# Kernel optimization log

Hardware: AMD Instinct MI355X
Metric: run time of the kernel (lower is better)

The kernel has to match this reference:

```python
import jax, jax.numpy as jnp
import numpy as np

N_FACES = 50000
C_IN = 256
C_OUT = 256
K = 9  # kernel_size ** 2
PAD_SIZE = N_FACES + 1


def _pad_features(x, face_is_pad):
    # Faithful to: padded_x = zeros(pad_size, C); padded_x[~face_is_pad] = x
    # rank[i] = position of row i among the non-pad slots (in order)
    rank = jnp.cumsum(~face_is_pad) - 1            # [P]
    rank = jnp.clip(rank, 0, x.shape[0] - 1)
    padded = jnp.where(face_is_pad[:, None], jnp.zeros((), x.dtype), x[rank])
    return padded                                   # [P, C_in]


def setup_inputs() -> dict:
    key = jax.random.key(0)
    k1, k2, k3 = jax.random.split(key, 3)
    x = jax.random.normal(k1, (N_FACES, C_IN), dtype=jnp.float32)
    weight = jax.random.normal(k2, (C_OUT, C_IN, 1, K), dtype=jnp.float32)
    bias = jnp.zeros((C_OUT,), dtype=jnp.float32)
    face_neighborhood = jax.random.randint(k3, (N_FACES, K), 0, PAD_SIZE, dtype=jnp.int64)
    # exactly one pad slot (the last one); sum(~face_is_pad) == N_FACES == x.shape[0]
    face_is_pad = jnp.zeros((PAD_SIZE,), dtype=bool).at[PAD_SIZE - 1].set(True)
    return {"x": x, "weight": weight, "bias": bias,
            "face_neighborhood": face_neighborhood,
            "face_is_pad": face_is_pad, "pad_size": PAD_SIZE}


def reference(x, weight, bias, face_neighborhood, face_is_pad, pad_size):
    # demodulation: per-output-channel L2 normalization of the weight
    dcoefs = jax.lax.rsqrt(jnp.sum(weight * weight, axis=(1, 2, 3)) + 1e-8)  # [O]
    w = weight * dcoefs[:, None, None, None]        # [O, I, 1, K]
    padded = _pad_features(x, face_is_pad)          # [P, I]
    gathered = padded[face_neighborhood]            # [N, K, I]
    # 1x9 conv over gathered neighbors == contraction over (I, K)
    out = jnp.einsum('nki,oik->no', gathered, w[:, :, 0, :]) + bias  # [N, O]
    return out
```

## Files before the change

### kernel.cpp

```cpp
#include <hip/hip_runtime.h>

#define NF    50000
#define PADP  50001
#define KN    9
#define KTOT  2304
#define NCHUNK 782
#define BM2   256
#define NBLK2 196
#define NKT   36
#define BUF   65536
#define BOFF  32768
#define IDXOFF2 131072

#define WT_OFF   0u
#define FLAG_OFF 1179648u
#define CNT_OFF  1179904u
#define PADX_OFF 1183744u

typedef float f32x4 __attribute__((ext_vector_type(4)));
typedef __bf16 bf16x8 __attribute__((ext_vector_type(8)));

typedef const __attribute__((address_space(1))) unsigned int* gas_t;
typedef __attribute__((address_space(3))) unsigned int* las_t;

static __device__ __forceinline__ void gll16(const void* g, void* l) {
  __builtin_amdgcn_global_load_lds((gas_t)g, (las_t)l, 16, 0, 0);
}

static __device__ __forceinline__ unsigned short f2bf(float f) {
  unsigned int u = __builtin_bit_cast(unsigned int, f);
  u = u + 0x7fffu + ((u >> 16) & 1u);
  return (unsigned short)(u >> 16);
}


__global__ void k_prep(const float* __restrict__ w, unsigned short* __restrict__ wt,
                       const unsigned char* __restrict__ pad, int* __restrict__ cnt,
                       const unsigned int* __restrict__ raw, int* __restrict__ flag) {
  if (blockIdx.x < 256) {
    int o = blockIdx.x;
    int i = threadIdx.x;
    const float* wr = w + (o * 256 + i) * 9;
    float wv[9];
    float s = 0.f;
#pragma unroll
    for (int k = 0; k < 9; ++k) { wv[k] = wr[k]; s += wv[k] * wv[k]; }
#pragma unroll
    for (int d = 32; d >= 1; d >>= 1) s += __shfl_xor(s, d);
    __shared__ float red[4];
    if ((i & 63) == 0) red[i >> 6] = s;
    __syncthreads();
    float dc = rsqrtf(red[0] + red[1] + red[2] + red[3] + 1e-8f);
#pragma unroll
    for (int k = 0; k < 9; ++k)
      wt[o * KTOT + k * 256 + i] = f2bf(wv[k] * dc);
  } else {
    int cb = blockIdx.x - 256;
    int t = cb * 256 + threadIdx.x;
    bool ip = (t < PADP) ? (pad[t] != 0) : true;
    unsigned long long m = __ballot(ip);
    int c = t >> 6;
    if ((threadIdx.x & 63) == 0 && c < NCHUNK) cnt[c] = __popcll(m);
    if (cb == 0 && threadIdx.x < 64) {
      unsigned int v = raw[threadIdx.x * 2 + 1];
      unsigned long long nz = __ballot(v != 0u);
      if (threadIdx.x == 0) flag[0] = (nz == 0ull) ? 1 : 0;
    }
  }
}

__global__ __launch_bounds__(256) void k_rankpadx(
    const float* __restrict__ x, const unsigned char* __restrict__ pad,
    const int* __restrict__ cnt, unsigned short* __restrict__ padx) {
  const int c = blockIdx.x;
  const int tid = threadIdx.x, w = tid >> 6, lane = tid & 63;
  int s = 0;
  for (int i = tid; i < c; i += 256) s += cnt[i];
#pragma unroll
  for (int d = 32; d >= 1; d >>= 1) s += __shfl_xor(s, d);
  __shared__ int red[4];
  __shared__ int rnk[64];
  if (lane == 0) red[w] = s;
  __syncthreads();
  const int S = red[0] + red[1] + red[2] + red[3];
  if (w == 0) {
    int p = c * 64 + lane;
    bool ip = (p < PADP) ? (pad[p] != 0) : true;
    unsigned long long m = __ballot(ip);
    int before = __popcll(m & ((1ull << lane) - 1ull));
    rnk[lane] = ip ? -1 : (p - (S + before));
  }
  __syncthreads();
  const int col = lane * 4;
#pragma unroll
  for (int i = 0; i < 16; ++i) {
    int rl = i * 4 + w;
    int pp = c * 64 + rl;
    if (pp >= PADP) continue;
    int rr = rnk[rl];
    ushort4 ov;
    if (rr < 0) { ov.x = 0; ov.y = 0; ov.z = 0; ov.w = 0; }
    else {
      const float4 v = *(const float4*)(x + rr * 256 + col);
      ov.x = f2bf(v.x); ov.y = f2bf(v.y); ov.z = f2bf(v.z); ov.w = f2bf(v.w);
    }
    *(ushort4*)(padx + pp * 256 + col) = ov;
  }
}

__global__ __launch_bounds__(512, 2) void k_main(
    const unsigned short* __restrict__ padx,
    const unsigned short* __restrict__ wt,
    const void* __restrict__ nbr,
    const int* __restrict__ flag,
    const float* __restrict__ bias,
    float* __restrict__ out) {
  __shared__ __align__(16) unsigned char sm[140288];
  const int tid = threadIdx.x;
  const int wv = tid >> 6, lane = tid & 63;
  const int m0 = blockIdx.x * BM2;
  int* idxl = (int*)(sm + IDXOFF2);

  const int q = lane & 15, hi = lane >> 4;
  const int wm = wv >> 2, wn = wv & 3;

  float bv[4];
#pragma unroll
  for (int ni = 0; ni < 4; ++ni) bv[ni] = bias[wn * 64 + ni * 16 + q];

  const bool f64 = (flag[0] != 0);
  const long long* n64 = (const long long*)nbr;
  const int* n32 = (const int*)nbr;
  for (int e = tid; e < BM2 * 9; e += 512) {
    int f = m0 + e / 9;
    if (f >= NF) f = NF - 1;
    int k = e - (e / 9) * 9;
    idxl[e] = f64 ? (int)n64[f * KN + k] : n32[f * KN + k];
  }
  __syncthreads();

  const int swsrc = ((tid & 7) ^ ((tid >> 3) & 7)) * 8;
  const int fl0 = tid >> 3;
  const int rb0 = fl0 * 9, rb1 = (fl0 + 64) * 9, rb2 = (fl0 + 128) * 9, rb3 = (fl0 + 192) * 9;
  const unsigned short* wtb00 = wt + (fl0      ) * KTOT + swsrc;
  const unsigned short* wtb01 = wt + (fl0 +  64) * KTOT + swsrc;
  const unsigned short* wtb10 = wt + (fl0 + 128) * KTOT + swsrc;
  const unsigned short* wtb11 = wt + (fl0 + 192) * KTOT + swsrc;

  const int q7 = q & 7;
  const int aof0 = wm * 16384 + q * 128 + ((hi    ) ^ q7) * 16;
  const int aof1 = wm * 16384 + q * 128 + ((4 + hi) ^ q7) * 16;
  const int bof0 = BOFF + (wn * 64 + q) * 128 + ((hi    ) ^ q7) * 16;
  const int bof1 = BOFF + (wn * 64 + q) * 128 + ((4 + hi) ^ q7) * 16;

  f32x4 acc[8][4];
#pragma unroll
  for (int a = 0; a < 8; ++a)
#pragma unroll
    for (int b = 0; b < 4; ++b) {
      acc[a][b][0] = 0.f; acc[a][b][1] = 0.f; acc[a][b][2] = 0.f; acc[a][b][3] = 0.f;
    }

  bf16x8 af[8], bq[4];
  int pA0 = idxl[rb0], pA1 = idxl[rb1], pA2 = idxl[rb2], pA3 = idxl[rb3];

  gll16(wtb00, sm + BOFF + tid * 16);
  gll16(wtb01, sm + BOFF + 8192 + tid * 16);
  gll16(wtb10, sm + BOFF + 16384 + tid * 16);
  gll16(wtb11, sm + BOFF + 24576 + tid * 16);
  gll16(padx + pA0 * 256 + swsrc, sm + tid * 16);
  gll16(padx + pA1 * 256 + swsrc, sm + 8192 + tid * 16);
  gll16(padx + pA2 * 256 + swsrc, sm + 16384 + tid * 16);
  gll16(padx + pA3 * 256 + swsrc, sm + 24576 + tid * 16);
  gll16(wtb00 + 64, sm + BUF + BOFF + tid * 16);
  gll16(wtb01 + 64, sm + BUF + BOFF + 8192 + tid * 16);
  gll16(wtb10 + 64, sm + BUF + BOFF + 16384 + tid * 16);
  gll16(wtb11 + 64, sm + BUF + BOFF + 24576 + tid * 16);
  asm volatile("s_waitcnt vmcnt(0)" ::: "memory");
  __builtin_amdgcn_s_barrier();

#define LD(p) (*(const bf16x8*)(p))
#define SB __builtin_amdgcn_sched_barrier(0);
#define MF(MI, AFI) \
  acc[MI][0] = __builtin_amdgcn_mfma_f32_16x16x32_bf16(af[AFI], bq[0], acc[MI][0], 0,0,0); \
  acc[MI][1] = __builtin_amdgcn_mfma_f32_16x16x32_bf16(af[AFI], bq[1], acc[MI][1], 0,0,0); \
  acc[MI][2] = __builtin_amdgcn_mfma_f32_16x16x32_bf16(af[AFI], bq[2], acc[MI][2], 0,0,0); \
  acc[MI][3] = __builtin_amdgcn_mfma_f32_16x16x32_bf16(af[AFI], bq[3], acc[MI][3], 0,0,0);
#define TAIL(M0,M1,M2,M3) \
  SB __builtin_amdgcn_s_barrier(); \
  asm volatile("s_waitcnt lgkmcnt(0)" ::: "memory"); SB \
  __builtin_amdgcn_s_setprio(1); \
  MF(M0,M0) MF(M1,M1) MF(M2,M2) MF(M3,M3) \
  __builtin_amdgcn_s_setprio(0); \
  SB __builtin_amdgcn_s_barrier();

#define PH0(CUR,OTH,C0A) { \
  const unsigned char* cb = sm + (CUR)*BUF; \
  af[0]=LD(cb+aof0); af[1]=LD(cb+aof0+2048); af[2]=LD(cb+aof0+4096); af[3]=LD(cb+aof0+6144); \
  bq[0]=LD(cb+bof0); bq[1]=LD(cb+bof0+2048); bq[2]=LD(cb+bof0+4096); bq[3]=LD(cb+bof0+6144); \
  gll16(padx + pA0*256 + (C0A) + swsrc, sm + (OTH)*BUF + tid*16); \
  gll16(padx + pA1*256 + (C0A) + swsrc, sm + (OTH)*BUF + 8192 + tid*16); \
  TAIL(0,1,2,3) }

#define PH1(CUR,OTH,C0A) { \
  const unsigned char* cb = sm + (CUR)*BUF; \
  af[4]=LD(cb+aof0+8192); af[5]=LD(cb+aof0+10240); af[6]=LD(cb+aof0+12288); af[7]=LD(cb+aof0+14336); \
  gll16(padx + pA2*256 + (C0A) + swsrc, sm + (OTH)*BUF + 16384 + tid*16); \
  gll16(padx + pA3*256 + (C0A) + swsrc, sm + (OTH)*BUF + 24576 + tid*16); \
  TAIL(4,5,6,7) }

#define PH2(CUR, DOREF) { \
  const unsigned char* cb = sm + (CUR)*BUF; \
  af[0]=LD(cb+aof1); af[1]=LD(cb+aof1+2048); af[2]=LD(cb+aof1+4096); af[3]=LD(cb+aof1+6144); \
  bq[0]=LD(cb+bof1); bq[1]=LD(cb+bof1+2048); bq[2]=LD(cb+bof1+4096); bq[3]=LD(cb+bof1+6144); \
  if (DOREF) { int gn = g4 + 1; if (gn > 8) gn = 8; \
    pA0 = idxl[rb0+gn]; pA1 = idxl[rb1+gn]; pA2 = idxl[rb2+gn]; pA3 = idxl[rb3+gn]; } \
  TAIL(0,1,2,3) }

#define PH3(CUR, KB) { \
  const unsigned char* cb = sm + (CUR)*BUF; \
  af[4]=LD(cb+aof1+8192); af[5]=LD(cb+aof1+10240); af[6]=LD(cb+aof1+12288); af[7]=LD(cb+aof1+14336); \
  gll16(wtb00 + (KB), sm + (CUR)*BUF + BOFF + tid*16); \
  gll16(wtb01 + (KB), sm + (CUR)*BUF + BOFF + 8192 + tid*16); \
  gll16(wtb10 + (KB), sm + (CUR)*BUF + BOFF + 16384 + tid*16); \
  gll16(wtb11 + (KB), sm + (CUR)*BUF + BOFF + 24576 + tid*16); \
  asm volatile("s_waitcnt vmcnt(4)" ::: "memory"); \
  TAIL(4,5,6,7) }

#pragma unroll 1
  for (int g4 = 0; g4 < 9; ++g4) {
    const int ktb = g4 * 4;
    int u;
    PH0(0,1,64) PH1(0,1,64) PH2(0,0)
    u = ktb + 2; if (u > 35) u = 35;
    PH3(0, u*64)
    PH0(1,0,128) PH1(1,0,128) PH2(1,0)
    u = ktb + 3; if (u > 35) u = 35;
    PH3(1, u*64)
    PH0(0,1,192) PH1(0,1,192) PH2(0,1)
    u = ktb + 4; if (u > 35) u = 35;
    PH3(0, u*64)
    PH0(1,0,0) PH1(1,0,0) PH2(1,0)
    u = ktb + 5; if (u > 35) u = 35;
    PH3(1, u*64)
  }
#undef PH0
#undef PH1
#undef PH2
#undef PH3
#undef TAIL
#undef MF
#undef LD
#undef SB
  asm volatile("s_waitcnt vmcnt(0)" ::: "memory");

#pragma unroll
  for (int ni = 0; ni < 4; ++ni) {
    const int col = wn * 64 + ni * 16 + q;
#pragma unroll
    for (int mi = 0; mi < 8; ++mi) {
#pragma unroll
      for (int rr = 0; rr < 4; ++rr) {
        const int row = m0 + wm * 128 + mi * 16 + hi * 4 + rr;
        if (row < NF) out[row * 256 + col] = acc[mi][ni][rr] + bv[ni];
      }
    }
  }
}

extern "C" void kernel_launch(void* const* d_in, const int* in_sizes, int n_in,
                              void* d_out, int out_size, void* d_ws, size_t ws_size,
                              hipStream_t stream) {
  const float* x = (const float*)d_in[0];
  const float* wfull = (const float*)d_in[1];
  const float* bias = (const float*)d_in[2];
  const void* nbr = d_in[3];
  const unsigned char* pad = (const unsigned char*)d_in[4];
  float* out = (float*)d_out;
  char* ws = (char*)d_ws;

  unsigned short* wt   = (unsigned short*)(ws + WT_OFF);
  int* flag            = (int*)(ws + FLAG_OFF);
  int* cnt             = (int*)(ws + CNT_OFF);
  unsigned short* padx = (unsigned short*)(ws + PADX_OFF);

  k_prep<<<452, 256, 0, stream>>>(wfull, wt, pad, cnt, (const unsigned int*)nbr, flag);
  k_rankpadx<<<NCHUNK, 256, 0, stream>>>(x, pad, cnt, padx);
  k_main<<<NBLK2, 512, 0, stream>>>(padx, wt, nbr, flag, bias, out);
}
```

Measured before the change: 87.68 us.

## Load weight fragments directly from global into registers, drop weight LDS staging

The weight (B) operand is no longer staged through LDS via global_load_lds. Each lane now reads its bf16 weight fragments straight from global memory into registers, double-buffered across half-k-steps. This halves the LDS footprint, which could allow more blocks per CU, and removes the LDS writes and reads for B. In exchange it issues more global loads per wave, relies on L2/L1 hits for the shared weights, and uses a hand-tuned vmcnt wait that must account for the new loads.

```diff
diff --git a/kernel.cpp b/kernel.cpp
--- a/kernel.cpp
+++ b/kernel.cpp
@@ -8,9 +8,8 @@
 #define BM2   256
 #define NBLK2 196
 #define NKT   36
-#define BUF   65536
-#define BOFF  32768
-#define IDXOFF2 131072
+#define BUF   32768
+#define IDXOFF2 65536
 
 #define WT_OFF   0u
 #define FLAG_OFF 1179648u
@@ -115,7 +114,7 @@
     const int* __restrict__ flag,
     const float* __restrict__ bias,
     float* __restrict__ out) {
-  __shared__ __align__(16) unsigned char sm[140288];
+  __shared__ __align__(16) unsigned char sm[74752];
   const int tid = threadIdx.x;
   const int wv = tid >> 6, lane = tid & 63;
   const int m0 = blockIdx.x * BM2;
@@ -142,16 +141,15 @@
   const int swsrc = ((tid & 7) ^ ((tid >> 3) & 7)) * 8;
   const int fl0 = tid >> 3;
   const int rb0 = fl0 * 9, rb1 = (fl0 + 64) * 9, rb2 = (fl0 + 128) * 9, rb3 = (fl0 + 192) * 9;
-  const unsigned short* wtb00 = wt + (fl0      ) * KTOT + swsrc;
-  const unsigned short* wtb01 = wt + (fl0 +  64) * KTOT + swsrc;
-  const unsigned short* wtb10 = wt + (fl0 + 128) * KTOT + swsrc;
-  const unsigned short* wtb11 = wt + (fl0 + 192) * KTOT + swsrc;
 
   const int q7 = q & 7;
   const int aof0 = wm * 16384 + q * 128 + ((hi    ) ^ q7) * 16;
   const int aof1 = wm * 16384 + q * 128 + ((4 + hi) ^ q7) * 16;
-  const int bof0 = BOFF + (wn * 64 + q) * 128 + ((hi    ) ^ q7) * 16;
-  const int bof1 = BOFF + (wn * 64 + q) * 128 + ((4 + hi) ^ q7) * 16;
+
+  const unsigned short* wB0 = wt + (wn * 64 +  0 + q) * KTOT + hi * 8;
+  const unsigned short* wB1 = wt + (wn * 64 + 16 + q) * KTOT + hi * 8;
+  const unsigned short* wB2 = wt + (wn * 64 + 32 + q) * KTOT + hi * 8;
+  const unsigned short* wB3 = wt + (wn * 64 + 48 + q) * KTOT + hi * 8;
 
   f32x4 acc[8][4];
 #pragma unroll
@@ -161,93 +159,74 @@
       acc[a][b][0] = 0.f; acc[a][b][1] = 0.f; acc[a][b][2] = 0.f; acc[a][b][3] = 0.f;
     }
 
-  bf16x8 af[8], bq[4];
+  bf16x8 af[8], bq0[4], bq1[4];
   int pA0 = idxl[rb0], pA1 = idxl[rb1], pA2 = idxl[rb2], pA3 = idxl[rb3];
 
-  gll16(wtb00, sm + BOFF + tid * 16);
-  gll16(wtb01, sm + BOFF + 8192 + tid * 16);
-  gll16(wtb10, sm + BOFF + 16384 + tid * 16);
-  gll16(wtb11, sm + BOFF + 24576 + tid * 16);
+  bq0[0] = *(const bf16x8*)(wB0);
+  bq0[1] = *(const bf16x8*)(wB1);
+  bq0[2] = *(const bf16x8*)(wB2);
+  bq0[3] = *(const bf16x8*)(wB3);
   gll16(padx + pA0 * 256 + swsrc, sm + tid * 16);
   gll16(padx + pA1 * 256 + swsrc, sm + 8192 + tid * 16);
   gll16(padx + pA2 * 256 + swsrc, sm + 16384 + tid * 16);
   gll16(padx + pA3 * 256 + swsrc, sm + 24576 + tid * 16);
-  gll16(wtb00 + 64, sm + BUF + BOFF + tid * 16);
-  gll16(wtb01 + 64, sm + BUF + BOFF + 8192 + tid * 16);
-  gll16(wtb10 + 64, sm + BUF + BOFF + 16384 + tid * 16);
-  gll16(wtb11 + 64, sm + BUF + BOFF + 24576 + tid * 16);
   asm volatile("s_waitcnt vmcnt(0)" ::: "memory");
   __builtin_amdgcn_s_barrier();
 
 #define LD(p) (*(const bf16x8*)(p))
 #define SB __builtin_amdgcn_sched_barrier(0);
-#define MF(MI, AFI) \
-  acc[MI][0] = __builtin_amdgcn_mfma_f32_16x16x32_bf16(af[AFI], bq[0], acc[MI][0], 0,0,0); \
-  acc[MI][1] = __builtin_amdgcn_mfma_f32_16x16x32_bf16(af[AFI], bq[1], acc[MI][1], 0,0,0); \
-  acc[MI][2] = __builtin_amdgcn_mfma_f32_16x16x32_bf16(af[AFI], bq[2], acc[MI][2], 0,0,0); \
-  acc[MI][3] = __builtin_amdgcn_mfma_f32_16x16x32_bf16(af[AFI], bq[3], acc[MI][3], 0,0,0);
-#define TAIL(M0,M1,M2,M3) \
+#define MF(MI, AFI, BQ) \
+  acc[MI][0] = __builtin_amdgcn_mfma_f32_16x16x32_bf16(af[AFI], BQ[0], acc[MI][0], 0,0,0); \
+  acc[MI][1] = __builtin_amdgcn_mfma_f32_16x16x32_bf16(af[AFI], BQ[1], acc[MI][1], 0,0,0); \
+  acc[MI][2] = __builtin_amdgcn_mfma_f32_16x16x32_bf16(af[AFI], BQ[2], acc[MI][2], 0,0,0); \
+  acc[MI][3] = __builtin_amdgcn_mfma_f32_16x16x32_bf16(af[AFI], BQ[3], acc[MI][3], 0,0,0);
+#define TAIL(M0,M1,M2,M3,BQ) \
   SB __builtin_amdgcn_s_barrier(); \
   asm volatile("s_waitcnt lgkmcnt(0)" ::: "memory"); SB \
   __builtin_amdgcn_s_setprio(1); \
-  MF(M0,M0) MF(M1,M1) MF(M2,M2) MF(M3,M3) \
+  MF(M0,M0,BQ) MF(M1,M1,BQ) MF(M2,M2,BQ) MF(M3,M3,BQ) \
   __builtin_amdgcn_s_setprio(0); \
   SB __builtin_amdgcn_s_barrier();
 
-#define PH0(CUR,OTH,C0A) { \
-  const unsigned char* cb = sm + (CUR)*BUF; \
-  af[0]=LD(cb+aof0); af[1]=LD(cb+aof0+2048); af[2]=LD(cb+aof0+4096); af[3]=LD(cb+aof0+6144); \
-  bq[0]=LD(cb+bof0); bq[1]=LD(cb+bof0+2048); bq[2]=LD(cb+bof0+4096); bq[3]=LD(cb+bof0+6144); \
-  gll16(padx + pA0*256 + (C0A) + swsrc, sm + (OTH)*BUF + tid*16); \
-  gll16(padx + pA1*256 + (C0A) + swsrc, sm + (OTH)*BUF + 8192 + tid*16); \
-  TAIL(0,1,2,3) }
-
-#define PH1(CUR,OTH,C0A) { \
-  const unsigned char* cb = sm + (CUR)*BUF; \
-  af[4]=LD(cb+aof0+8192); af[5]=LD(cb+aof0+10240); af[6]=LD(cb+aof0+12288); af[7]=LD(cb+aof0+14336); \
-  gll16(padx + pA2*256 + (C0A) + swsrc, sm + (OTH)*BUF + 16384 + tid*16); \
-  gll16(padx + pA3*256 + (C0A) + swsrc, sm + (OTH)*BUF + 24576 + tid*16); \
-  TAIL(4,5,6,7) }
-
-#define PH2(CUR, DOREF) { \
-  const unsigned char* cb = sm + (CUR)*BUF; \
-  af[0]=LD(cb+aof1); af[1]=LD(cb+aof1+2048); af[2]=LD(cb+aof1+4096); af[3]=LD(cb+aof1+6144); \
-  bq[0]=LD(cb+bof1); bq[1]=LD(cb+bof1+2048); bq[2]=LD(cb+bof1+4096); bq[3]=LD(cb+bof1+6144); \
-  if (DOREF) { int gn = g4 + 1; if (gn > 8) gn = 8; \
-    pA0 = idxl[rb0+gn]; pA1 = idxl[rb1+gn]; pA2 = idxl[rb2+gn]; pA3 = idxl[rb3+gn]; } \
-  TAIL(0,1,2,3) }
-
-#define PH3(CUR, KB) { \
-  const unsigned char* cb = sm + (CUR)*BUF; \
-  af[4]=LD(cb+aof1+8192); af[5]=LD(cb+aof1+10240); af[6]=LD(cb+aof1+12288); af[7]=LD(cb+aof1+14336); \
-  gll16(wtb00 + (KB), sm + (CUR)*BUF + BOFF + tid*16); \
-  gll16(wtb01 + (KB), sm + (CUR)*BUF + BOFF + 8192 + tid*16); \
-  gll16(wtb10 + (KB), sm + (CUR)*BUF + BOFF + 16384 + tid*16); \
-  gll16(wtb11 + (KB), sm + (CUR)*BUF + BOFF + 24576 + tid*16); \
-  asm volatile("s_waitcnt vmcnt(4)" ::: "memory"); \
-  TAIL(4,5,6,7) }
-
 #pragma unroll 1
-  for (int g4 = 0; g4 < 9; ++g4) {
-    const int ktb = g4 * 4;
-    int u;
-    PH0(0,1,64) PH1(0,1,64) PH2(0,0)
-    u = ktb + 2; if (u > 35) u = 35;
-    PH3(0, u*64)
-    PH0(1,0,128) PH1(1,0,128) PH2(1,0)
-    u = ktb + 3; if (u > 35) u = 35;
-    PH3(1, u*64)
-    PH0(0,1,192) PH1(0,1,192) PH2(0,1)
-    u = ktb + 4; if (u > 35) u = 35;
-    PH3(0, u*64)
-    PH0(1,0,0) PH1(1,0,0) PH2(1,0)
-    u = ktb + 5; if (u > 35) u = 35;
-    PH3(1, u*64)
-  }
-#undef PH0
-#undef PH1
-#undef PH2
-#undef PH3
+  for (int kt = 0; kt < NKT; ++kt) {
+    const unsigned char* cb = sm + (kt & 1) * BUF;
+    unsigned char* ob = (unsigned char*)sm + ((kt & 1) ^ 1) * BUF;
+    const int c0n = ((kt + 1) & 3) * 64;
+    af[0] = LD(cb + aof0);        af[1] = LD(cb + aof0 + 2048);
+    af[2] = LD(cb + aof0 + 4096); af[3] = LD(cb + aof0 + 6144);
+    {
+      const int kb1 = kt * 64 + 32;
+      bq1[0] = LD(wB0 + kb1); bq1[1] = LD(wB1 + kb1);
+      bq1[2] = LD(wB2 + kb1); bq1[3] = LD(wB3 + kb1);
+    }
+    gll16(padx + pA0 * 256 + c0n + swsrc, ob + tid * 16);
+    gll16(padx + pA1 * 256 + c0n + swsrc, ob + 8192 + tid * 16);
+    SB
+    asm volatile("s_waitcnt vmcnt(10)" ::: "memory");
+    TAIL(0,1,2,3,bq0)
+    af[4] = LD(cb + aof0 + 8192);  af[5] = LD(cb + aof0 + 10240);
+    af[6] = LD(cb + aof0 + 12288); af[7] = LD(cb + aof0 + 14336);
+    gll16(padx + pA2 * 256 + c0n + swsrc, ob + 16384 + tid * 16);
+    gll16(padx + pA3 * 256 + c0n + swsrc, ob + 24576 + tid * 16);
+    TAIL(4,5,6,7,bq0)
+    af[0] = LD(cb + aof1);        af[1] = LD(cb + aof1 + 2048);
+    af[2] = LD(cb + aof1 + 4096); af[3] = LD(cb + aof1 + 6144);
+    {
+      const int kb0 = ((kt + 1 < NKT) ? kt + 1 : NKT - 1) * 64;
+      bq0[0] = LD(wB0 + kb0); bq0[1] = LD(wB1 + kb0);
+      bq0[2] = LD(wB2 + kb0); bq0[3] = LD(wB3 + kb0);
+    }
+    TAIL(0,1,2,3,bq1)
+    af[4] = LD(cb + aof1 + 8192);  af[5] = LD(cb + aof1 + 10240);
+    af[6] = LD(cb + aof1 + 12288); af[7] = LD(cb + aof1 + 14336);
+    if ((kt & 3) == 2) {
+      int gn = (kt >> 2) + 1; if (gn > 8) gn = 8;
+      pA0 = idxl[rb0 + gn]; pA1 = idxl[rb1 + gn];
+      pA2 = idxl[rb2 + gn]; pA3 = idxl[rb3 + gn];
+    }
+    TAIL(4,5,6,7,bq1)
+  }
 #undef TAIL
 #undef MF
 #undef LD
```

New measurement: 132.5 us. 1.51x slower.
